# Kernel tuning notes

Hardware: AMD Instinct MI355X
Metric: run time of the kernel (lower is better)

## Reference

```python
import math
import jax, jax.numpy as jnp
import numpy as np

B, T, G, E, H, L = 8, 32, 32, 768, 12, 4
S = T * G
HD = E // H


def setup_inputs() -> dict:
    key = jax.random.key(0)
    ks = jax.random.split(key, 10)
    def n(k, shape, s=0.02):
        return s * jax.random.normal(k, shape, jnp.float32)
    return dict(
        x=jax.random.normal(ks[0], (B, T, G, E), jnp.float32),
        study_date=jnp.sort(jax.random.randint(ks[1], (B, T), 0, 50), axis=-1),
        wpe=n(ks[2], (50, E)),
        ln1_w=jnp.ones((L, E)), ln1_b=jnp.zeros((L, E)),
        in_w=n(ks[3], (L, 3 * E, E)), in_b=jnp.zeros((L, 3 * E)),
        out_w=n(ks[4], (L, E, E)), out_b=jnp.zeros((L, E)),
        ln2_w=jnp.ones((L, E)), ln2_b=jnp.zeros((L, E)),
        fc_w=n(ks[5], (L, 4 * E, E)), fc_b=jnp.zeros((L, 4 * E)),
        proj_w=n(ks[6], (L, E, 4 * E), 0.02 / math.sqrt(2 * L)),
        proj_b=jnp.zeros((L, E)),
        lnf_w=jnp.ones((E,)), lnf_b=jnp.zeros((E,)),
    )


def _ln(x, w, b):
    m = x.mean(-1, keepdims=True)
    v = ((x - m) ** 2).mean(-1, keepdims=True)
    return (x - m) / jnp.sqrt(v + 1e-5) * w + b


def _gelu_new(x):
    # NewGELU: 0.5*x*(1+tanh(sqrt(2/pi)*(x+0.044715*x^3)))
    c = np.sqrt(2.0 / np.pi).astype(np.float32)
    return 0.5 * x * (1.0 + jnp.tanh(c * (x + 0.044715 * x ** 3)))


def _mask_bias():
    # block-causal mask: tril over T blocks, each expanded to G x G
    allowed = jnp.tril(jnp.ones((T, T), bool))
    allowed = jnp.repeat(jnp.repeat(allowed, G, axis=0), G, axis=1)  # [S,S]
    return jnp.where(allowed, 0.0, -jnp.inf).astype(jnp.float32)


def reference(x, study_date, wpe, ln1_w, ln1_b, in_w, in_b, out_w, out_b,
              ln2_w, ln2_b, fc_w, fc_b, proj_w, proj_b, lnf_w, lnf_b):
    b, t, g, d = x.shape
    s = t * g
    pos = wpe[jnp.clip(study_date, 0, 49)]  # [B,T,E]
    pos = jnp.broadcast_to(pos[:, :, None, :], (b, t, g, d)).reshape(b, s, d)
    h = x.reshape(b, s, d) + pos
    bias = _mask_bias()  # [S,S]
    inv_sqrt_hd = 1.0 / np.sqrt(HD).astype(np.float32)
    for l in range(L):
        y = _ln(h, ln1_w[l], ln1_b[l])
        qkv = y @ in_w[l].T + in_b[l]  # [B,S,3E]
        q, k, v = jnp.split(qkv, 3, axis=-1)
        q = q.reshape(b, s, H, HD).transpose(0, 2, 1, 3)
        k = k.reshape(b, s, H, HD).transpose(0, 2, 1, 3)
        v = v.reshape(b, s, H, HD).transpose(0, 2, 1, 3)
        att = jnp.einsum('bhqd,bhkd->bhqk', q, k) * inv_sqrt_hd + bias
        att = jax.nn.softmax(att, axis=-1)
        o = jnp.einsum('bhqk,bhkd->bhqd', att, v)
        o = o.transpose(0, 2, 1, 3).reshape(b, s, d)
        h = h + o @ out_w[l].T + out_b[l]
        y2 = _ln(h, ln2_w[l], ln2_b[l])
        h = h + _gelu_new(y2 @ fc_w[l].T + fc_b[l]) @ proj_w[l].T + proj_b[l]
    return _ln(h, lnf_w, lnf_b)
```

## Files before the change

### kernel.cpp

```cpp
#include <hip/hip_runtime.h>
#include <hip/hip_bf16.h>

typedef __attribute__((ext_vector_type(8))) __bf16 bf16x8;
typedef __attribute__((ext_vector_type(4))) float f32x4;

typedef unsigned short u16;

__device__ __forceinline__ u16 f2bf(float f) {
    unsigned int u = __float_as_uint(f);
    u += 0x7FFFu + ((u >> 16) & 1u);
    return (u16)(u >> 16);
}

__device__ __forceinline__ void g2l16(const void* g, void* l) {
    __builtin_amdgcn_global_load_lds(
        (const __attribute__((address_space(1))) void*)g,
        (__attribute__((address_space(3))) void*)l, 16, 0, 0);
}

#define BB 8
#define SS 1024
#define EE 768
#define HH 12
#define HD 64
#define LL 4

__global__ __launch_bounds__(256) void cvt_k(const float* __restrict__ in,
                                             u16* __restrict__ out, int n4) {
    for (int i = blockIdx.x * 256 + threadIdx.x; i < n4; i += gridDim.x * 256) {
        float4 v = ((const float4*)in)[i];
        ushort4 u;
        u.x = f2bf(v.x); u.y = f2bf(v.y); u.z = f2bf(v.z); u.w = f2bf(v.w);
        ((ushort4*)out)[i] = u;
    }
}

__global__ __launch_bounds__(256) void embed_k(const float* __restrict__ x,
                                               const int* __restrict__ sd,
                                               const float* __restrict__ wpe,
                                               float* __restrict__ h) {
    int idx = blockIdx.x * 256 + threadIdx.x;
    int e4 = idx % 192;
    int bs = idx / 192;
    int b = bs >> 10;
    int t = (bs >> 5) & 31;
    int date = sd[b * 32 + t];
    date = date < 0 ? 0 : (date > 49 ? 49 : date);
    float4 xv = ((const float4*)x)[idx];
    float4 pv = ((const float4*)wpe)[date * 192 + e4];
    float4 r; r.x = xv.x + pv.x; r.y = xv.y + pv.y; r.z = xv.z + pv.z; r.w = xv.w + pv.w;
    ((float4*)h)[idx] = r;
}

template <bool BF16OUT>
__global__ __launch_bounds__(256) void ln_k(const float* __restrict__ in,
                                            const float* __restrict__ w,
                                            const float* __restrict__ b,
                                            void* __restrict__ out) {
    int tid = threadIdx.x, wv = tid >> 6, lane = tid & 63;
    int token = blockIdx.x * 4 + wv;
    const float4* ip = (const float4*)(in + (size_t)token * EE);
    float4 v[3];
#pragma unroll
    for (int p = 0; p < 3; p++) v[p] = ip[p * 64 + lane];
    float s = 0.f;
#pragma unroll
    for (int p = 0; p < 3; p++) s += v[p].x + v[p].y + v[p].z + v[p].w;
#pragma unroll
    for (int m = 1; m < 64; m <<= 1) s += __shfl_xor(s, m);
    float mean = s * (1.f / 768.f);
    float vs = 0.f;
#pragma unroll
    for (int p = 0; p < 3; p++) {
        float dx = v[p].x - mean, dy = v[p].y - mean, dz = v[p].z - mean, dw = v[p].w - mean;
        vs += dx * dx + dy * dy + dz * dz + dw * dw;
    }
#pragma unroll
    for (int m = 1; m < 64; m <<= 1) vs += __shfl_xor(vs, m);
    float rstd = rsqrtf(vs * (1.f / 768.f) + 1e-5f);
    const float4* wp = (const float4*)w;
    const float4* bp = (const float4*)b;
#pragma unroll
    for (int p = 0; p < 3; p++) {
        float4 wv4 = wp[p * 64 + lane], bv4 = bp[p * 64 + lane];
        float rx = (v[p].x - mean) * rstd * wv4.x + bv4.x;
        float ry = (v[p].y - mean) * rstd * wv4.y + bv4.y;
        float rz = (v[p].z - mean) * rstd * wv4.z + bv4.z;
        float rw = (v[p].w - mean) * rstd * wv4.w + bv4.w;
        if (BF16OUT) {
            ushort4 u; u.x = f2bf(rx); u.y = f2bf(ry); u.z = f2bf(rz); u.w = f2bf(rw);
            ((ushort4*)((u16*)out + (size_t)token * EE))[p * 64 + lane] = u;
        } else {
            float4 r; r.x = rx; r.y = ry; r.z = rz; r.w = rw;
            ((float4*)((float*)out + (size_t)token * EE))[p * 64 + lane] = r;
        }
    }
}

template <int MODE, int BM>
__global__ __launch_bounds__(256) void gemm_bt(const u16* __restrict__ A,
                                               const u16* __restrict__ Bw,
                                               const float* __restrict__ bias,
                                               float* __restrict__ hres,
                                               u16* __restrict__ outb,
                                               u16* __restrict__ vT,
                                               u16* __restrict__ kT,
                                               int M, int N, int K) {
    constexpr int TM = BM / 32;
    constexpr int NST = (BM == 128) ? 3 : 4;
    constexpr int PD = NST - 2;
    constexpr int ATILE = BM * 32;
    constexpr int TILE = ATILE + 4096;
    constexpr int SSTR = TILE * 2;
    __shared__ u16 SM[NST * TILE];

    const int tid = threadIdx.x;
    const int lane = tid & 63, w = tid >> 6;
    const int quad = lane >> 4, l16 = lane & 15;

    const int nx = N >> 7;
    const int ny = M / BM;
    const int id = blockIdx.x;
    const int xcd = id & 7, s = id >> 3;
    const int yt = xcd * (ny >> 3) + s / nx;
    const int xt = s % nx;
    const int m0 = yt * BM, n0 = xt * 128;
    const int wm = (w >> 1) * (BM / 2), wn = (w & 1) * 64;

    f32x4 acc[TM][4];
#pragma unroll
    for (int i = 0; i < TM; i++)
#pragma unroll
        for (int j = 0; j < 4; j++) acc[i][j] = (f32x4){0.f, 0.f, 0.f, 0.f};

    const int swz = (quad ^ ((l16 >> 1) & 3)) * 8;
    const int nk = K >> 5;

    const int cB0 = w * 128 + lane, cB1 = cB0 + 64;
    const int rB0 = cB0 >> 2, gB0 = (((cB0 & 3) ^ ((cB0 >> 3) & 3)) * 8);
    const int rB1 = cB1 >> 2, gB1 = (((cB1 & 3) ^ ((cB1 >> 3) & 3)) * 8);
    const u16* Bp0 = Bw + (size_t)(n0 + rB0) * K + gB0;
    const u16* Bp1 = Bw + (size_t)(n0 + rB1) * K + gB1;
    char* lB0 = (char*)SM + ATILE * 2 + w * 2048;
    char* lB1 = lB0 + 1024;
    const int cA0 = (BM == 128) ? cB0 : tid;
    const int rA0 = cA0 >> 2, gA0 = (((cA0 & 3) ^ ((cA0 >> 3) & 3)) * 8);
    const u16* Ap0 = A + (size_t)(m0 + rA0) * K + gA0;
    char* lA0 = (char*)SM + ((BM == 128) ? w * 2048 : w * 1024);
    const int cA1 = cB1;
    const int rA1 = cA1 >> 2, gA1 = (((cA1 & 3) ^ ((cA1 >> 3) & 3)) * 8);
    const u16* Ap1 = A + (size_t)(m0 + rA1) * K + gA1;
    char* lA1 = (char*)SM + w * 2048 + 1024;

    g2l16(Ap0, lA0);
    if (BM == 128) g2l16(Ap1, lA1);
    g2l16(Bp0, lB0);
    g2l16(Bp1, lB1);
    if (PD == 2) {
        g2l16(Ap0 + 32, lA0 + SSTR);
        if (BM == 128) g2l16(Ap1 + 32, lA1 + SSTR);
        g2l16(Bp0 + 32, lB0 + SSTR);
        g2l16(Bp1 + 32, lB1 + SSTR);
    }

    int rb = 0, wb = PD;
    for (int ki = 0; ki < nk; ki++) {
        if (ki + PD < nk) {
            const int kb = (ki + PD) << 5;
            const int bo = wb * SSTR;
            g2l16(Ap0 + kb, lA0 + bo);
            if (BM == 128) g2l16(Ap1 + kb, lA1 + bo);
            g2l16(Bp0 + kb, lB0 + bo);
            g2l16(Bp1 + kb, lB1 + bo);
        }
        if (BM == 128) {
            if (ki < nk - 1) __builtin_amdgcn_s_waitcnt(0x0F74);
            else             __builtin_amdgcn_s_waitcnt(0x0F70);
        } else {
            if (ki < nk - 2)      __builtin_amdgcn_s_waitcnt(0x0F76);
            else if (ki == nk - 2) __builtin_amdgcn_s_waitcnt(0x0F73);
            else                  __builtin_amdgcn_s_waitcnt(0x0F70);
        }
        __builtin_amdgcn_s_barrier();

        const u16* Ab = (const u16*)SM + rb * TILE;
        const u16* Bb = Ab + ATILE;
        bf16x8 af[TM], bfr[4];
#pragma unroll
        for (int t = 0; t < TM; t++)
            af[t] = *(const bf16x8*)(Ab + (wm + t * 16 + l16) * 32 + swz);
#pragma unroll
        for (int t = 0; t < 4; t++)
            bfr[t] = *(const bf16x8*)(Bb + (wn + t * 16 + l16) * 32 + swz);
#pragma unroll
        for (int tm = 0; tm < TM; tm++)
#pragma unroll
            for (int tn = 0; tn < 4; tn++)
                acc[tm][tn] = __builtin_amdgcn_mfma_f32_16x16x32_bf16(
                    af[tm], bfr[tn], acc[tm][tn], 0, 0, 0);
        rb = (rb + 1 == NST) ? 0 : rb + 1;
        wb = (wb + 1 == NST) ? 0 : wb + 1;
    }

#pragma unroll
    for (int tm = 0; tm < TM; tm++) {
        int rowm = m0 + wm + tm * 16 + quad * 4;
#pragma unroll
        for (int tn = 0; tn < 4; tn++) {
            int coln = n0 + wn + tn * 16 + l16;
            float bv = bias[coln];
            f32x4 v = acc[tm][tn];
            if (MODE == 0) {
                int b = rowm >> 10, s2 = rowm & 1023;
                if (coln < EE) {
                    int hh = coln >> 6, d = coln & 63;
                    u16* qp = outb + ((size_t)(b * HH + hh) * SS + s2) * HD + d;
#pragma unroll
                    for (int r = 0; r < 4; r++) qp[r * HD] = f2bf(v[r] + bv);
                } else if (coln < 2 * EE) {
                    int hh = (coln - EE) >> 6, d = (coln - EE) & 63;
                    u16* kp = kT + ((size_t)(b * HH + hh) * SS + s2) * HD + d;
#pragma unroll
                    for (int r = 0; r < 4; r++) kp[r * HD] = f2bf(v[r] + bv);
                } else {
                    int hh = (coln - 2 * EE) >> 6, d = (coln - 2 * EE) & 63;
                    ushort4 pk;
                    pk.x = f2bf(v[0] + bv); pk.y = f2bf(v[1] + bv);
                    pk.z = f2bf(v[2] + bv); pk.w = f2bf(v[3] + bv);
                    *(ushort4*)(vT + (((size_t)((b * HH + hh) * HD + d)) << 10) + s2) = pk;
                }
            } else if (MODE == 1) {
#pragma unroll
                for (int r = 0; r < 4; r++) {
                    size_t idx = (size_t)(rowm + r) * N + coln;
                    hres[idx] += v[r] + bv;
                }
            } else {
#pragma unroll
                for (int r = 0; r < 4; r++) {
                    float x = v[r] + bv;
                    float t = x + 0.044715f * x * x * x;
                    float e = __expf(-1.5957691216057308f * t);
                    float th = (1.f - e) / (1.f + e);
                    outb[(size_t)(rowm + r) * N + coln] = f2bf(0.5f * x * (1.f + th));
                }
            }
        }
    }
}

__global__ __launch_bounds__(256) void attn_k(const u16* __restrict__ qT,
                                              const u16* __restrict__ kT,
                                              const u16* __restrict__ vT,
                                              u16* __restrict__ o) {
    __shared__ u16 Ks[2048];
    __shared__ u16 Vs[2048];
    __shared__ u16 P[4][16 * 40];
    int tid = threadIdx.x, w = tid >> 6, lane = tid & 63;
    int quad = lane >> 4, l16 = lane & 15;
    int blk = blockIdx.x;
    int qg = 15 - (blk / 96);
    int bh = blk % 96;
    int b = bh / HH, hh = bh % HH;
    int q0 = qg * 64;
    int kend_blk = q0 + 64;
    int kend_w = q0 + ((w >> 1) ? 64 : 32);

    const u16* qbase = qT + ((size_t)bh * SS + q0 + w * 16 + l16) * HD + quad * 8;
    bf16x8 qf0 = *(const bf16x8*)(qbase);
    bf16x8 qf1 = *(const bf16x8*)(qbase + 32);

    f32x4 of[4];
#pragma unroll
    for (int i = 0; i < 4; i++) of[i] = (f32x4){0.f, 0.f, 0.f, 0.f};
    float mrun[4], lrun[4];
#pragma unroll
    for (int r = 0; r < 4; r++) { mrun[r] = -__builtin_inff(); lrun[r] = 0.f; }

    int tK = tid >> 3, dcK = ((tid & 7) ^ (tK & 7));
    const u16* kg = kT + ((size_t)bh * SS + tK) * HD + dcK * 8;
    char* kl = (char*)Ks + w * 1024;
    int dV = tid >> 2, tcV = ((tid & 3) ^ ((dV >> 1) & 3));
    const u16* vg = vT + ((size_t)bh * HD + dV) * SS + tcV * 8;
    char* vl = (char*)Vs + w * 1024;
    u16* Pw = P[w];

    for (int kb = 0; kb < kend_blk; kb += 32) {
        g2l16(kg + (size_t)kb * HD, kl);
        g2l16(vg + kb, vl);
        __syncthreads();
        if (kb < kend_w) {
            int t0 = l16, t1 = 16 + l16;
            bf16x8 k00 = *(const bf16x8*)(Ks + (t0 * 8 + (quad ^ (l16 & 7))) * 8);
            bf16x8 k01 = *(const bf16x8*)(Ks + (t0 * 8 + ((4 + quad) ^ (l16 & 7))) * 8);
            bf16x8 k10 = *(const bf16x8*)(Ks + (t1 * 8 + (quad ^ (l16 & 7))) * 8);
            bf16x8 k11 = *(const bf16x8*)(Ks + (t1 * 8 + ((4 + quad) ^ (l16 & 7))) * 8);
            f32x4 s0 = (f32x4){0.f, 0.f, 0.f, 0.f};
            f32x4 s1 = (f32x4){0.f, 0.f, 0.f, 0.f};
            s0 = __builtin_amdgcn_mfma_f32_16x16x32_bf16(qf0, k00, s0, 0, 0, 0);
            s0 = __builtin_amdgcn_mfma_f32_16x16x32_bf16(qf1, k01, s0, 0, 0, 0);
            s1 = __builtin_amdgcn_mfma_f32_16x16x32_bf16(qf0, k10, s1, 0, 0, 0);
            s1 = __builtin_amdgcn_mfma_f32_16x16x32_bf16(qf1, k11, s1, 0, 0, 0);

            float alpha[4];
#pragma unroll
            for (int r = 0; r < 4; r++) {
                float a0 = s0[r] * 0.125f, a1 = s1[r] * 0.125f;
                float mx = fmaxf(a0, a1);
#pragma unroll
                for (int m = 1; m < 16; m <<= 1) mx = fmaxf(mx, __shfl_xor(mx, m));
                float mnew = fmaxf(mrun[r], mx);
                alpha[r] = __expf(mrun[r] - mnew);
                float p0 = __expf(a0 - mnew);
                float p1 = __expf(a1 - mnew);
                float ps = p0 + p1;
#pragma unroll
                for (int m = 1; m < 16; m <<= 1) ps += __shfl_xor(ps, m);
                lrun[r] = lrun[r] * alpha[r] + ps;
                mrun[r] = mnew;
                Pw[(quad * 4 + r) * 40 + l16] = f2bf(p0);
                Pw[(quad * 4 + r) * 40 + 16 + l16] = f2bf(p1);
            }
#pragma unroll
            for (int n4 = 0; n4 < 4; n4++) {
                of[n4][0] *= alpha[0]; of[n4][1] *= alpha[1];
                of[n4][2] *= alpha[2]; of[n4][3] *= alpha[3];
            }
            bf16x8 pf = *(const bf16x8*)(Pw + l16 * 40 + quad * 8);
#pragma unroll
            for (int n4 = 0; n4 < 4; n4++) {
                int d = n4 * 16 + l16;
                bf16x8 vf = *(const bf16x8*)(Vs + (d * 4 + (quad ^ ((d >> 1) & 3))) * 8);
                of[n4] = __builtin_amdgcn_mfma_f32_16x16x32_bf16(pf, vf, of[n4], 0, 0, 0);
            }
        }
        __syncthreads();
    }

    float inv[4];
#pragma unroll
    for (int r = 0; r < 4; r++) inv[r] = 1.f / lrun[r];
#pragma unroll
    for (int n4 = 0; n4 < 4; n4++)
#pragma unroll
        for (int r = 0; r < 4; r++)
            o[(size_t)(b * SS + q0 + w * 16 + quad * 4 + r) * EE + hh * HD + n4 * 16 + l16] =
                f2bf(of[n4][r] * inv[r]);
}

extern "C" void kernel_launch(void* const* d_in, const int* in_sizes, int n_in,
                              void* d_out, int out_size, void* d_ws, size_t ws_size,
                              hipStream_t stream) {
    const float* x     = (const float*)d_in[0];
    const int*   sd    = (const int*)d_in[1];
    const float* wpe   = (const float*)d_in[2];
    const float* ln1w  = (const float*)d_in[3];
    const float* ln1b  = (const float*)d_in[4];
    const float* in_w  = (const float*)d_in[5];
    const float* in_b  = (const float*)d_in[6];
    const float* out_w = (const float*)d_in[7];
    const float* out_b = (const float*)d_in[8];
    const float* ln2w  = (const float*)d_in[9];
    const float* ln2b  = (const float*)d_in[10];
    const float* fc_w  = (const float*)d_in[11];
    const float* fc_b  = (const float*)d_in[12];
    const float* pr_w  = (const float*)d_in[13];
    const float* pr_b  = (const float*)d_in[14];
    const float* lnfw  = (const float*)d_in[15];
    const float* lnfb  = (const float*)d_in[16];
    float* outp = (float*)d_out;

    char* ws = (char*)d_ws;
    float* h   = (float*)ws;
    u16* ybuf  = (u16*)(ws + 25165824);
    u16* big   = (u16*)(ws + 37748736);
    u16* qT    = big;
    u16* kT    = big + 6291456;
    u16* vT    = (u16*)(ws + 88080384);
    u16* wb    = (u16*)(ws + 100663296);
    u16* w_in  = wb;
    u16* w_out = w_in + 7077888;
    u16* w_fc  = w_out + 2359296;
    u16* w_pr  = w_fc + 9437184;

    cvt_k<<<1024, 256, 0, stream>>>(in_w,  w_in,  7077888 / 4);
    cvt_k<<<1024, 256, 0, stream>>>(out_w, w_out, 2359296 / 4);
    cvt_k<<<1024, 256, 0, stream>>>(fc_w,  w_fc,  9437184 / 4);
    cvt_k<<<1024, 256, 0, stream>>>(pr_w,  w_pr,  9437184 / 4);
    embed_k<<<6144, 256, 0, stream>>>(x, sd, wpe, h);

    for (int l = 0; l < LL; l++) {
        ln_k<true><<<2048, 256, 0, stream>>>(h, ln1w + l * EE, ln1b + l * EE, ybuf);
        gemm_bt<0, 128><<<18 * 64, 256, 0, stream>>>(
            ybuf, w_in + (size_t)l * 2304 * 768, in_b + l * 2304, nullptr, qT, vT, kT,
            8192, 2304, 768);
        attn_k<<<1536, 256, 0, stream>>>(qT, kT, vT, ybuf);
        gemm_bt<1, 64><<<6 * 128, 256, 0, stream>>>(
            ybuf, w_out + (size_t)l * 768 * 768, out_b + l * 768, h, nullptr, nullptr, nullptr,
            8192, 768, 768);
        ln_k<true><<<2048, 256, 0, stream>>>(h, ln2w + l * EE, ln2b + l * EE, ybuf);
        gemm_bt<2, 128><<<24 * 64, 256, 0, stream>>>(
            ybuf, w_fc + (size_t)l * 3072 * 768, fc_b + l * 3072, nullptr, big, nullptr, nullptr,
            8192, 3072, 768);
        gemm_bt<1, 128><<<6 * 64, 256, 0, stream>>>(
            big, w_pr + (size_t)l * 768 * 3072, pr_b + l * 768, h, nullptr, nullptr, nullptr,
            8192, 768, 3072);
    }
    ln_k<false><<<2048, 256, 0, stream>>>(h, lnfw, lnfb, outp);
}
```

Before: 1.283 ms.

## Compute transposed attention scores to keep P in registers and skip LDS round-trip

Attention now computes S^T = K·Q^T so each lane holds a full column of scores for one query. Softmax reductions then need only two cross-quad shuffles, and the probabilities can be packed straight into the MFMA A operand without going through shared memory. The V layout written by the QKV GEMM epilogue is permuted within each 32-token block so the register P ordering lines up with V. It also adds a lazy rescale that only updates the running max when it grows by more than 8, which saves exp/rescale work but lets exponents drift above the true max, a small numerical risk.

Result: faster. 1.159 ms (-9.6%).

```diff
diff --git a/kernel.cpp b/kernel.cpp
--- a/kernel.cpp
+++ b/kernel.cpp
@@ -5,6 +5,7 @@
 typedef __attribute__((ext_vector_type(4))) float f32x4;
 
 typedef unsigned short u16;
+typedef __attribute__((ext_vector_type(8))) u16 u16x8;
 
 __device__ __forceinline__ u16 f2bf(float f) {
     unsigned int u = __float_as_uint(f);
@@ -224,10 +225,13 @@
                     for (int r = 0; r < 4; r++) kp[r * HD] = f2bf(v[r] + bv);
                 } else {
                     int hh = (coln - 2 * EE) >> 6, d = (coln - 2 * EE) & 63;
+                    int j0 = s2 & 31;
+                    int k0 = (j0 < 16) ? ((j0 >> 2) * 8) : (((j0 - 16) >> 2) * 8 + 4);
+                    int s2p = (s2 & ~31) | k0;
                     ushort4 pk;
                     pk.x = f2bf(v[0] + bv); pk.y = f2bf(v[1] + bv);
                     pk.z = f2bf(v[2] + bv); pk.w = f2bf(v[3] + bv);
-                    *(ushort4*)(vT + (((size_t)((b * HH + hh) * HD + d)) << 10) + s2) = pk;
+                    *(ushort4*)(vT + (((size_t)((b * HH + hh) * HD + d)) << 10) + s2p) = pk;
                 }
             } else if (MODE == 1) {
 #pragma unroll
@@ -255,7 +259,6 @@
                                               u16* __restrict__ o) {
     __shared__ u16 Ks[2048];
     __shared__ u16 Vs[2048];
-    __shared__ u16 P[4][16 * 40];
     int tid = threadIdx.x, w = tid >> 6, lane = tid & 63;
     int quad = lane >> 4, l16 = lane & 15;
     int blk = blockIdx.x;
@@ -273,9 +276,7 @@
     f32x4 of[4];
 #pragma unroll
     for (int i = 0; i < 4; i++) of[i] = (f32x4){0.f, 0.f, 0.f, 0.f};
-    float mrun[4], lrun[4];
-#pragma unroll
-    for (int r = 0; r < 4; r++) { mrun[r] = -__builtin_inff(); lrun[r] = 0.f; }
+    float mrun = -__builtin_inff(), lrun = 0.f;
 
     int tK = tid >> 3, dcK = ((tid & 7) ^ (tK & 7));
     const u16* kg = kT + ((size_t)bh * SS + tK) * HD + dcK * 8;
@@ -283,7 +284,6 @@
     int dV = tid >> 2, tcV = ((tid & 3) ^ ((dV >> 1) & 3));
     const u16* vg = vT + ((size_t)bh * HD + dV) * SS + tcV * 8;
     char* vl = (char*)Vs + w * 1024;
-    u16* Pw = P[w];
 
     for (int kb = 0; kb < kend_blk; kb += 32) {
         g2l16(kg + (size_t)kb * HD, kl);
@@ -295,57 +295,69 @@
             bf16x8 k01 = *(const bf16x8*)(Ks + (t0 * 8 + ((4 + quad) ^ (l16 & 7))) * 8);
             bf16x8 k10 = *(const bf16x8*)(Ks + (t1 * 8 + (quad ^ (l16 & 7))) * 8);
             bf16x8 k11 = *(const bf16x8*)(Ks + (t1 * 8 + ((4 + quad) ^ (l16 & 7))) * 8);
-            f32x4 s0 = (f32x4){0.f, 0.f, 0.f, 0.f};
-            f32x4 s1 = (f32x4){0.f, 0.f, 0.f, 0.f};
-            s0 = __builtin_amdgcn_mfma_f32_16x16x32_bf16(qf0, k00, s0, 0, 0, 0);
-            s0 = __builtin_amdgcn_mfma_f32_16x16x32_bf16(qf1, k01, s0, 0, 0, 0);
-            s1 = __builtin_amdgcn_mfma_f32_16x16x32_bf16(qf0, k10, s1, 0, 0, 0);
-            s1 = __builtin_amdgcn_mfma_f32_16x16x32_bf16(qf1, k11, s1, 0, 0, 0);
-
-            float alpha[4];
+            f32x4 sT0 = (f32x4){0.f, 0.f, 0.f, 0.f};
+            f32x4 sT1 = (f32x4){0.f, 0.f, 0.f, 0.f};
+            sT0 = __builtin_amdgcn_mfma_f32_16x16x32_bf16(k00, qf0, sT0, 0, 0, 0);
+            sT0 = __builtin_amdgcn_mfma_f32_16x16x32_bf16(k01, qf1, sT0, 0, 0, 0);
+            sT1 = __builtin_amdgcn_mfma_f32_16x16x32_bf16(k10, qf0, sT1, 0, 0, 0);
+            sT1 = __builtin_amdgcn_mfma_f32_16x16x32_bf16(k11, qf1, sT1, 0, 0, 0);
+
+            float a0[4], a1[4];
+#pragma unroll
+            for (int r = 0; r < 4; r++) { a0[r] = sT0[r] * 0.125f; a1[r] = sT1[r] * 0.125f; }
+            float mx = fmaxf(fmaxf(fmaxf(a0[0], a0[1]), fmaxf(a0[2], a0[3])),
+                             fmaxf(fmaxf(a1[0], a1[1]), fmaxf(a1[2], a1[3])));
+            mx = fmaxf(mx, __shfl_xor(mx, 16));
+            mx = fmaxf(mx, __shfl_xor(mx, 32));
+            if (!__all(mx - mrun <= 8.0f)) {
+                float mnew = fmaxf(mrun, mx);
+                float alpha = __expf(mrun - mnew);
+                mrun = mnew;
+                lrun *= alpha;
+                float al[4];
+#pragma unroll
+                for (int r = 0; r < 4; r++) al[r] = __shfl(alpha, quad * 4 + r);
+#pragma unroll
+                for (int n4 = 0; n4 < 4; n4++) {
+                    of[n4][0] *= al[0]; of[n4][1] *= al[1];
+                    of[n4][2] *= al[2]; of[n4][3] *= al[3];
+                }
+            }
+            float p0[4], p1[4];
 #pragma unroll
             for (int r = 0; r < 4; r++) {
-                float a0 = s0[r] * 0.125f, a1 = s1[r] * 0.125f;
-                float mx = fmaxf(a0, a1);
-#pragma unroll
-                for (int m = 1; m < 16; m <<= 1) mx = fmaxf(mx, __shfl_xor(mx, m));
-                float mnew = fmaxf(mrun[r], mx);
-                alpha[r] = __expf(mrun[r] - mnew);
-                float p0 = __expf(a0 - mnew);
-                float p1 = __expf(a1 - mnew);
-                float ps = p0 + p1;
-#pragma unroll
-                for (int m = 1; m < 16; m <<= 1) ps += __shfl_xor(ps, m);
-                lrun[r] = lrun[r] * alpha[r] + ps;
-                mrun[r] = mnew;
-                Pw[(quad * 4 + r) * 40 + l16] = f2bf(p0);
-                Pw[(quad * 4 + r) * 40 + 16 + l16] = f2bf(p1);
+                p0[r] = __expf(a0[r] - mrun);
+                p1[r] = __expf(a1[r] - mrun);
             }
-#pragma unroll
-            for (int n4 = 0; n4 < 4; n4++) {
-                of[n4][0] *= alpha[0]; of[n4][1] *= alpha[1];
-                of[n4][2] *= alpha[2]; of[n4][3] *= alpha[3];
-            }
-            bf16x8 pf = *(const bf16x8*)(Pw + l16 * 40 + quad * 8);
+            float ps = ((p0[0] + p0[1]) + (p0[2] + p0[3])) +
+                       ((p1[0] + p1[1]) + (p1[2] + p1[3]));
+            ps += __shfl_xor(ps, 16);
+            ps += __shfl_xor(ps, 32);
+            lrun += ps;
+            union { u16x8 u; bf16x8 v; } pa;
+            pa.u[0] = f2bf(p0[0]); pa.u[1] = f2bf(p0[1]);
+            pa.u[2] = f2bf(p0[2]); pa.u[3] = f2bf(p0[3]);
+            pa.u[4] = f2bf(p1[0]); pa.u[5] = f2bf(p1[1]);
+            pa.u[6] = f2bf(p1[2]); pa.u[7] = f2bf(p1[3]);
 #pragma unroll
             for (int n4 = 0; n4 < 4; n4++) {
                 int d = n4 * 16 + l16;
                 bf16x8 vf = *(const bf16x8*)(Vs + (d * 4 + (quad ^ ((d >> 1) & 3))) * 8);
-                of[n4] = __builtin_amdgcn_mfma_f32_16x16x32_bf16(pf, vf, of[n4], 0, 0, 0);
+                of[n4] = __builtin_amdgcn_mfma_f32_16x16x32_bf16(pa.v, vf, of[n4], 0, 0, 0);
             }
         }
         __syncthreads();
     }
 
-    float inv[4];
-#pragma unroll
-    for (int r = 0; r < 4; r++) inv[r] = 1.f / lrun[r];
+    float linv[4];
+#pragma unroll
+    for (int r = 0; r < 4; r++) linv[r] = 1.f / __shfl(lrun, quad * 4 + r);
 #pragma unroll
     for (int n4 = 0; n4 < 4; n4++)
 #pragma unroll
         for (int r = 0; r < 4; r++)
             o[(size_t)(b * SS + q0 + w * 16 + quad * 4 + r) * EE + hh * HD + n4 * 16 + l16] =
-                f2bf(of[n4][r] * inv[r]);
+                f2bf(of[n4][r] * linv[r]);
 }
 
 extern "C" void kernel_launch(void* const* d_in, const int* in_sizes, int n_in,
```
